# Optimization experiments

Hardware: AMD Instinct MI355X
Metric: run time of the kernel (lower is better)

Reference implementation:

```python
import jax, jax.numpy as jnp
import numpy as np


def setup_inputs() -> dict:
    key = jax.random.key(0)
    contour = jax.random.uniform(key, (200, 2), dtype=jnp.float32)  # coords in [0,1]
    return {"contour": contour, "size": 384}


def reference(contour, size):
    S = size
    eps = 1e-05
    k = 100000.0  # forward hardcodes k, ignoring self.k
    # mesh: (S^2, 1, 2), normalized pixel coordinates (torch.meshgrid default 'ij')
    grid = jnp.stack(jnp.meshgrid(jnp.arange(S), jnp.arange(S), indexing="ij"), axis=-1)
    mesh = (grid.reshape(-1, 2).astype(jnp.float32) / S)[:, None, :]
    diff = contour[None, :, :] - mesh                      # (S^2, N, 2)
    norm_diff = jnp.linalg.norm(diff, axis=-1)             # (S^2, N)
    min_diff = jnp.min(norm_diff, axis=1).reshape(S, S)    # distance to nearest vertex
    roll_diff = jnp.roll(diff, -1, axis=1)                 # next vertex diff
    # torch.roll(roll_diff, 1, dims=2) on a size-2 axis swaps x/y components
    cross = diff * roll_diff[..., ::-1]                    # (S^2, N, 2)
    sign = jnp.tanh(k * (cross[..., 1] - cross[..., 0]))   # smooth sign of 2D cross
    nd = jnp.clip(norm_diff, eps)
    nr = jnp.clip(jnp.linalg.norm(roll_diff, axis=-1), eps)
    cos_ang = jnp.clip(jnp.sum(diff * roll_diff, axis=-1) / (nd * nr), -1.0 + eps, 1.0 - eps)
    angles = jnp.arccos(cos_ang)                           # (S^2, N)
    winding = jnp.sum(sign * angles, axis=1) / (2.0 * jnp.pi)  # (S^2,)
    resize = winding.reshape(1, S, S)
    prod = resize * min_diff                               # (1, S, S)
    dmap = (prod / jnp.max(prod))[None]                    # (1, 1, S, S)
    return dmap
```

## Files before the change

kernel.cpp:

```cpp
#include <hip/hip_runtime.h>
#include <math.h>


#define INV_2PI 0.15915494309189535f
#define TWO_PI  6.28318530717958648f
#define PI_F    3.14159265358979323846f
#define HPI_F   1.57079632679489662f
#define KK2     200000.0f
#define CTHR    9e-5f

__device__ __forceinline__ float atan01(float q) {
    const float z = q * q;
    float p = fmaf(z,  0.0208351f, -0.0851330f);
    p = fmaf(z, p,  0.1801410f);
    p = fmaf(z, p, -0.3302995f);
    p = fmaf(z, p,  0.9998660f);
    return q * p;
}

__device__ __forceinline__ float corr_term(float ax_, float ay_, float bx_,
                                           float by_, float px, float py,
                                           float V) {
    const float dxc = ax_ - px, dyc = ay_ - py;
    const float dxn = bx_ - px, dyn = by_ - py;
    const float dot = fmaf(dxc, dxn, dyc * dyn);
    const float ay = fabsf(V), ax = fabsf(dot);
    const float mn = fminf(ax, ay), mx = fmaxf(ax, ay);
    const float q  = mn * __builtin_amdgcn_rcpf(fmaxf(mx, 1e-30f));
    float an = atan01(q);
    an = (ay > ax)    ? (HPI_F - an) : an;
    an = (dot < 0.0f) ? (PI_F - an)  : an;
    const float e = __expf(ay * -KK2);
    const float t = (1.0f - e) * __builtin_amdgcn_rcpf(1.0f + e);
    return (1.0f - t) * copysignf(an, -V);
}

__global__ void __launch_bounds__(256)
scan_kernel(const float2* __restrict__ c, int N, int S, float invS,
            float* __restrict__ wbuf) {
    __shared__ int   D[512];
    __shared__ float WC[512];
    __shared__ int   lst[16];
    __shared__ int   lcnt;

    const int tid = threadIdx.x;
    const int col = blockIdx.x;
    const float px = (float)col * invS;
    const float Sf = (float)S;

    for (int t = tid; t < 512; t += 256) { D[t] = 0; WC[t] = 0.0f; }
    if (tid == 0) lcnt = 0;
    __syncthreads();

    for (int n = tid; n < N; n += 256) {
        const float2 a = c[n];
        const float2 b = c[(n + 1 < N) ? (n + 1) : 0];
        const float EX = b.x - a.x;
        const float EY = b.y - a.y;
        const float Cc = a.x * b.y - a.y * b.x;
        const float W  = fmaf(-px, EY, Cc);

        const float ylo = fminf(a.y, b.y);
        const float yhi = fmaxf(a.y, b.y);
        const int s = (b.y > a.y) ? 1 : -1;
        int ja = (int)ceilf(ylo * Sf);
        int jb = (int)ceilf(yhi * Sf);
        ja = max(ja, 0); jb = min(jb, S);
        if (ja < jb) {
            const float Ga = (float)s * fmaf(EX, (float)ja * invS, W);
            const float Gb = (float)s * fmaf(EX, (float)(jb - 1) * invS, W);
            int j0 = ja, j1 = jb;
            if (Ga > 0.0f && Gb > 0.0f) {
            } else if (!(Ga > 0.0f) && !(Gb > 0.0f)) {
                j1 = j0;
            } else {
                const float r = -W / EX;
                const float rj = fminf(fmaxf(r * Sf, -1.0f), 386.0f);
                int jm = (int)ceilf(rj);
                jm = min(max(jm, ja), jb);
                if (Ga > 0.0f) j1 = jm; else j0 = jm;
            }
            if (j0 < j1) {
                atomicAdd(&D[j0],  s);
                atomicAdd(&D[j1], -s);
            }
        }

        const float aEX = fabsf(EX);
        if (aEX < 1e-12f) {
            if (fabsf(W) < CTHR) {
                const int k = atomicAdd(&lcnt, 1);
                if (k < 16) lst[k] = n;
            }
        } else {
            const float r  = -W / EX;
            const float dl = CTHR / aEX;
            float flo = (r - dl) * Sf;
            float fhi = (r + dl) * Sf;
            if (fhi >= 0.0f && flo <= Sf - 1.0f) {
                flo = fmaxf(flo, 0.0f);
                fhi = fminf(fhi, Sf - 1.0f);
                const int jl = (int)ceilf(flo);
                const int jh = (int)floorf(fhi);
                if (jh - jl > 12) {
                    const int k = atomicAdd(&lcnt, 1);
                    if (k < 16) lst[k] = n;
                } else {
                    for (int j = jl; j <= jh; ++j) {
                        const float py = (float)j * invS;
                        const float V = fmaf(EX, py, W);
                        if (fabsf(V) < CTHR)
                            atomicAdd(&WC[j],
                                      corr_term(a.x, a.y, b.x, b.y, px, py, V));
                    }
                }
            }
        }
    }
    __syncthreads();

    const int L = min(lcnt, 16);
    for (int k = 0; k < L; ++k) {
        const int n = lst[k];
        const float2 a = c[n];
        const float2 b = c[(n + 1 < N) ? (n + 1) : 0];
        const float EX = b.x - a.x;
        const float EY = b.y - a.y;
        const float W  = fmaf(-px, EY, a.x * b.y - a.y * b.x);
        for (int j = tid; j < S; j += 256) {
            const float py = (float)j * invS;
            const float V = fmaf(EX, py, W);
            if (fabsf(V) < CTHR)
                atomicAdd(&WC[j], corr_term(a.x, a.y, b.x, b.y, px, py, V));
        }
    }
    __syncthreads();

    #pragma unroll
    for (int off = 1; off < 512; off <<= 1) {
        const int j0 = tid, j1 = tid + 256;
        const int v0 = D[j0] + ((j0 >= off) ? D[j0 - off] : 0);
        const int v1 = D[j1] + ((j1 >= off) ? D[j1 - off] : 0);
        __syncthreads();
        D[j0] = v0; D[j1] = v1;
        __syncthreads();
    }

    for (int j = tid; j < S; j += 256)
        wbuf[col * S + j] = fmaf(-TWO_PI, (float)D[j], -WC[j]);
}

__global__ void __launch_bounds__(256)
prod_kernel(const float2* __restrict__ c, int N, int S, float invS,
            const float* __restrict__ wbuf, float* __restrict__ out,
            float* __restrict__ bmax) {
    __shared__ float2 sv[256];
    __shared__ int    scnt;
    __shared__ float  s_cd[4];
    __shared__ float  s_red[4];

    const int tid  = threadIdx.x;
    const int lane = tid & 63;
    const int wid  = tid >> 6;

    const int nbx = S >> 4;
    const int bi = blockIdx.x / nbx;
    const int bj = blockIdx.x - bi * nbx;
    const int i = (bi << 4) + (tid >> 4);
    const int j = (bj << 4) + (tid & 15);
    const float px = (float)i * invS, py = (float)j * invS;

    const float cx = ((float)(bi << 4) + 7.5f) * invS;
    const float cy = ((float)(bj << 4) + 7.5f) * invS;

    float cmin = 1e30f;
    for (int n = tid; n < N; n += 256) {
        const float2 v = c[n];
        const float dx = v.x - cx, dy = v.y - cy;
        cmin = fminf(cmin, fmaf(dx, dx, dy * dy));
    }
    #pragma unroll
    for (int off = 32; off >= 1; off >>= 1)
        cmin = fminf(cmin, __shfl_down(cmin, off, 64));
    if (lane == 0) s_cd[wid] = cmin;
    if (tid == 0) scnt = 0;
    __syncthreads();
    const float minc = fminf(fminf(s_cd[0], s_cd[1]), fminf(s_cd[2], s_cd[3]));

    const float T  = sqrtf(minc) + 0.0560f;
    const float T2 = T * T;

    for (int n = tid; n < N; n += 256) {
        const float2 v = c[n];
        const float dx = v.x - cx, dy = v.y - cy;
        if (fmaf(dx, dx, dy * dy) <= T2) {
            const int k = atomicAdd(&scnt, 1);
            sv[k] = v;
        }
    }
    __syncthreads();

    const int M = scnt;
    float minn = 1e30f;
    for (int k = 0; k < M; ++k) {
        const float2 v = sv[k];
        const float dx = v.x - px, dy = v.y - py;
        minn = fminf(minn, fmaf(dx, dx, dy * dy));
    }

    const int p = i * S + j;
    const float prod = (wbuf[p] * INV_2PI) * __builtin_amdgcn_sqrtf(minn);
    out[p] = prod;

    float v = prod;
    #pragma unroll
    for (int off = 32; off >= 1; off >>= 1)
        v = fmaxf(v, __shfl_down(v, off, 64));
    if (lane == 0) s_red[wid] = v;
    __syncthreads();
    if (tid == 0)
        bmax[blockIdx.x] = fmaxf(fmaxf(s_red[0], s_red[1]),
                                 fmaxf(s_red[2], s_red[3]));
}

__global__ void __launch_bounds__(256)
normalize_kernel(float4* __restrict__ out4, const float* __restrict__ bmax,
                 int nmax, int total4) {
    const int tid  = threadIdx.x;
    const int lane = tid & 63;
    const int wid  = tid >> 6;

    float m = -INFINITY;
    for (int t = tid; t < nmax; t += 256) m = fmaxf(m, bmax[t]);
    #pragma unroll
    for (int off = 32; off >= 1; off >>= 1)
        m = fmaxf(m, __shfl_down(m, off, 64));
    __shared__ float sm[4];
    if (lane == 0) sm[wid] = m;
    __syncthreads();
    m = fmaxf(fmaxf(sm[0], sm[1]), fmaxf(sm[2], sm[3]));
    const float inv = 1.0f / m;

    const int idx = blockIdx.x * 256 + tid;
    if (idx < total4) {
        float4 v = out4[idx];
        v.x *= inv; v.y *= inv; v.z *= inv; v.w *= inv;
        out4[idx] = v;
    }
}

extern "C" void kernel_launch(void* const* d_in, const int* in_sizes, int n_in,
                              void* d_out, int out_size, void* d_ws, size_t ws_size,
                              hipStream_t stream) {
    const float2* contour = (const float2*)d_in[0];
    const int N = in_sizes[0] / 2;
    const int S = (int)(sqrt((double)out_size) + 0.5);
    const float invS = 1.0f / (float)S;
    float* out  = (float*)d_out;
    float* bmax = (float*)d_ws;
    float* wbuf = (float*)((char*)d_ws + 16384);

    scan_kernel<<<S, 256, 0, stream>>>(contour, N, S, invS, wbuf);

    const int total  = S * S;
    const int pblocks = total / 256;
    prod_kernel<<<pblocks, 256, 0, stream>>>(contour, N, S, invS, wbuf,
                                             out, bmax);

    const int total4  = total / 4;
    const int nblocks = (total4 + 255) / 256;
    normalize_kernel<<<nblocks, 256, 0, stream>>>((float4*)out, bmax,
                                                  pblocks, total4);
}
```

Before: 64.21 us.

## Shrink scan kernel to single wavefront with shuffle-based prefix sum

The per-column scan kernel now runs with one 64-lane wavefront instead of 256 threads. The 18-barrier shared-memory Hillis-Steele scan over 512 entries is replaced by a per-lane sequential sum over 6 elements plus a wavefront shuffle scan, so only the two initial barriers remain. The threshold for deferring near-edge corrections to the cooperative list is raised to match the narrower block. The new layout hardcodes 6 entries per lane, so it assumes S is at most 384, and each block now walks the 200 edges with four times fewer threads.

```diff
diff --git a/kernel.cpp b/kernel.cpp
--- a/kernel.cpp
+++ b/kernel.cpp
@@ -35,24 +35,25 @@
     return (1.0f - t) * copysignf(an, -V);
 }
 
-__global__ void __launch_bounds__(256)
+__global__ void __launch_bounds__(64)
 scan_kernel(const float2* __restrict__ c, int N, int S, float invS,
             float* __restrict__ wbuf) {
-    __shared__ int   D[512];
-    __shared__ float WC[512];
+    __shared__ int   D[448];
+    __shared__ float WC[384];
     __shared__ int   lst[16];
     __shared__ int   lcnt;
 
-    const int tid = threadIdx.x;
-    const int col = blockIdx.x;
+    const int lane = threadIdx.x;
+    const int col  = blockIdx.x;
     const float px = (float)col * invS;
     const float Sf = (float)S;
 
-    for (int t = tid; t < 512; t += 256) { D[t] = 0; WC[t] = 0.0f; }
-    if (tid == 0) lcnt = 0;
-    __syncthreads();
-
-    for (int n = tid; n < N; n += 256) {
+    for (int t = lane; t < 448; t += 64) D[t] = 0;
+    for (int t = lane; t < 384; t += 64) WC[t] = 0.0f;
+    if (lane == 0) lcnt = 0;
+    __syncthreads();
+
+    for (int n = lane; n < N; n += 64) {
         const float2 a = c[n];
         const float2 b = c[(n + 1 < N) ? (n + 1) : 0];
         const float EX = b.x - a.x;
@@ -102,7 +103,7 @@
                 fhi = fminf(fhi, Sf - 1.0f);
                 const int jl = (int)ceilf(flo);
                 const int jh = (int)floorf(fhi);
-                if (jh - jl > 12) {
+                if (jh - jl > 24) {
                     const int k = atomicAdd(&lcnt, 1);
                     if (k < 16) lst[k] = n;
                 } else {
@@ -127,7 +128,7 @@
         const float EX = b.x - a.x;
         const float EY = b.y - a.y;
         const float W  = fmaf(-px, EY, a.x * b.y - a.y * b.x);
-        for (int j = tid; j < S; j += 256) {
+        for (int j = lane; j < S; j += 64) {
             const float py = (float)j * invS;
             const float V = fmaf(EX, py, W);
             if (fabsf(V) < CTHR)
@@ -136,18 +137,26 @@
     }
     __syncthreads();
 
-    #pragma unroll
-    for (int off = 1; off < 512; off <<= 1) {
-        const int j0 = tid, j1 = tid + 256;
-        const int v0 = D[j0] + ((j0 >= off) ? D[j0 - off] : 0);
-        const int v1 = D[j1] + ((j1 >= off) ? D[j1 - off] : 0);
-        __syncthreads();
-        D[j0] = v0; D[j1] = v1;
-        __syncthreads();
-    }
-
-    for (int j = tid; j < S; j += 256)
-        wbuf[col * S + j] = fmaf(-TWO_PI, (float)D[j], -WC[j]);
+    int d0 = D[6 * lane + 0], d1 = D[6 * lane + 1], d2 = D[6 * lane + 2];
+    int d3 = D[6 * lane + 3], d4 = D[6 * lane + 4], d5 = D[6 * lane + 5];
+    const int l0 = d0,      l1 = l0 + d1, l2 = l1 + d2;
+    const int l3 = l2 + d3, l4 = l3 + d4, l5 = l4 + d5;
+    int inc = l5;
+    #pragma unroll
+    for (int off = 1; off < 64; off <<= 1) {
+        const int y = __shfl_up(inc, off, 64);
+        if (lane >= off) inc += y;
+    }
+    const int excl = inc - l5;
+
+    const int jb6 = 6 * lane;
+    float* wrow = wbuf + col * S + jb6;
+    wrow[0] = fmaf(-TWO_PI, (float)(excl + l0), -WC[jb6 + 0]);
+    wrow[1] = fmaf(-TWO_PI, (float)(excl + l1), -WC[jb6 + 1]);
+    wrow[2] = fmaf(-TWO_PI, (float)(excl + l2), -WC[jb6 + 2]);
+    wrow[3] = fmaf(-TWO_PI, (float)(excl + l3), -WC[jb6 + 3]);
+    wrow[4] = fmaf(-TWO_PI, (float)(excl + l4), -WC[jb6 + 4]);
+    wrow[5] = fmaf(-TWO_PI, (float)(excl + l5), -WC[jb6 + 5]);
 }
 
 __global__ void __launch_bounds__(256)
@@ -260,7 +269,7 @@
     float* bmax = (float*)d_ws;
     float* wbuf = (float*)((char*)d_ws + 16384);
 
-    scan_kernel<<<S, 256, 0, stream>>>(contour, N, S, invS, wbuf);
+    scan_kernel<<<S, 64, 0, stream>>>(contour, N, S, invS, wbuf);
 
     const int total  = S * S;
     const int pblocks = total / 256;
```

New measurement: 66.02 us. +2.8%, slower.

## Fuse per-column winding scan into tiled product kernel, dropping intermediate buffer

Applied to the files above, without the earlier changes.

Merges the per-column winding-number scan kernel into the 16x16 tile kernel. Each tile now computes its own crossing differences and correction terms for its 16 columns, clipped to its 16 rows, and prefix-sums them in shared memory. The contour is staged once in LDS. This removes one launch and the global winding buffer round trip. In exchange, every tile re-walks all edges for its columns (16 rows of 16 threads per edge pass), which duplicates edge work across row tiles. It also assumes N<=256 for the shared staging.

```diff
diff --git a/kernel.cpp b/kernel.cpp
--- a/kernel.cpp
+++ b/kernel.cpp
@@ -35,125 +35,12 @@
     return (1.0f - t) * copysignf(an, -V);
 }
 
-__global__ void __launch_bounds__(256)
-scan_kernel(const float2* __restrict__ c, int N, int S, float invS,
-            float* __restrict__ wbuf) {
-    __shared__ int   D[512];
-    __shared__ float WC[512];
-    __shared__ int   lst[16];
-    __shared__ int   lcnt;
-
-    const int tid = threadIdx.x;
-    const int col = blockIdx.x;
-    const float px = (float)col * invS;
-    const float Sf = (float)S;
-
-    for (int t = tid; t < 512; t += 256) { D[t] = 0; WC[t] = 0.0f; }
-    if (tid == 0) lcnt = 0;
-    __syncthreads();
-
-    for (int n = tid; n < N; n += 256) {
-        const float2 a = c[n];
-        const float2 b = c[(n + 1 < N) ? (n + 1) : 0];
-        const float EX = b.x - a.x;
-        const float EY = b.y - a.y;
-        const float Cc = a.x * b.y - a.y * b.x;
-        const float W  = fmaf(-px, EY, Cc);
-
-        const float ylo = fminf(a.y, b.y);
-        const float yhi = fmaxf(a.y, b.y);
-        const int s = (b.y > a.y) ? 1 : -1;
-        int ja = (int)ceilf(ylo * Sf);
-        int jb = (int)ceilf(yhi * Sf);
-        ja = max(ja, 0); jb = min(jb, S);
-        if (ja < jb) {
-            const float Ga = (float)s * fmaf(EX, (float)ja * invS, W);
-            const float Gb = (float)s * fmaf(EX, (float)(jb - 1) * invS, W);
-            int j0 = ja, j1 = jb;
-            if (Ga > 0.0f && Gb > 0.0f) {
-            } else if (!(Ga > 0.0f) && !(Gb > 0.0f)) {
-                j1 = j0;
-            } else {
-                const float r = -W / EX;
-                const float rj = fminf(fmaxf(r * Sf, -1.0f), 386.0f);
-                int jm = (int)ceilf(rj);
-                jm = min(max(jm, ja), jb);
-                if (Ga > 0.0f) j1 = jm; else j0 = jm;
-            }
-            if (j0 < j1) {
-                atomicAdd(&D[j0],  s);
-                atomicAdd(&D[j1], -s);
-            }
-        }
-
-        const float aEX = fabsf(EX);
-        if (aEX < 1e-12f) {
-            if (fabsf(W) < CTHR) {
-                const int k = atomicAdd(&lcnt, 1);
-                if (k < 16) lst[k] = n;
-            }
-        } else {
-            const float r  = -W / EX;
-            const float dl = CTHR / aEX;
-            float flo = (r - dl) * Sf;
-            float fhi = (r + dl) * Sf;
-            if (fhi >= 0.0f && flo <= Sf - 1.0f) {
-                flo = fmaxf(flo, 0.0f);
-                fhi = fminf(fhi, Sf - 1.0f);
-                const int jl = (int)ceilf(flo);
-                const int jh = (int)floorf(fhi);
-                if (jh - jl > 12) {
-                    const int k = atomicAdd(&lcnt, 1);
-                    if (k < 16) lst[k] = n;
-                } else {
-                    for (int j = jl; j <= jh; ++j) {
-                        const float py = (float)j * invS;
-                        const float V = fmaf(EX, py, W);
-                        if (fabsf(V) < CTHR)
-                            atomicAdd(&WC[j],
-                                      corr_term(a.x, a.y, b.x, b.y, px, py, V));
-                    }
-                }
-            }
-        }
-    }
-    __syncthreads();
-
-    const int L = min(lcnt, 16);
-    for (int k = 0; k < L; ++k) {
-        const int n = lst[k];
-        const float2 a = c[n];
-        const float2 b = c[(n + 1 < N) ? (n + 1) : 0];
-        const float EX = b.x - a.x;
-        const float EY = b.y - a.y;
-        const float W  = fmaf(-px, EY, a.x * b.y - a.y * b.x);
-        for (int j = tid; j < S; j += 256) {
-            const float py = (float)j * invS;
-            const float V = fmaf(EX, py, W);
-            if (fabsf(V) < CTHR)
-                atomicAdd(&WC[j], corr_term(a.x, a.y, b.x, b.y, px, py, V));
-        }
-    }
-    __syncthreads();
-
-    #pragma unroll
-    for (int off = 1; off < 512; off <<= 1) {
-        const int j0 = tid, j1 = tid + 256;
-        const int v0 = D[j0] + ((j0 >= off) ? D[j0 - off] : 0);
-        const int v1 = D[j1] + ((j1 >= off) ? D[j1 - off] : 0);
-        __syncthreads();
-        D[j0] = v0; D[j1] = v1;
-        __syncthreads();
-    }
-
-    for (int j = tid; j < S; j += 256)
-        wbuf[col * S + j] = fmaf(-TWO_PI, (float)D[j], -WC[j]);
-}
-
-__global__ void __launch_bounds__(256)
-prod_kernel(const float2* __restrict__ c, int N, int S, float invS,
-            const float* __restrict__ wbuf, float* __restrict__ out,
-            float* __restrict__ bmax) {
+__global__ void __launch_bounds__(256, 4)
+tile_kernel(const float2* __restrict__ c, int N, int S, float invS,
+            float* __restrict__ out, float* __restrict__ bmax) {
+    __shared__ float2 sc[256];
+    __shared__ int    D[16][17];
+    __shared__ float  WC[16][16];
     __shared__ float2 sv[256];
     __shared__ int    scnt;
     __shared__ float  s_cd[4];
@@ -162,36 +49,110 @@
     const int tid  = threadIdx.x;
     const int lane = tid & 63;
     const int wid  = tid >> 6;
+    const float Sf = (float)S;
 
     const int nbx = S >> 4;
     const int bi = blockIdx.x / nbx;
     const int bj = blockIdx.x - bi * nbx;
-    const int i = (bi << 4) + (tid >> 4);
-    const int j = (bj << 4) + (tid & 15);
+    const int i0 = bi << 4;
+    const int jt = bj << 4;
+
+    if (tid < N) sc[tid] = c[tid];
+    for (int t = tid; t < 272; t += 256) ((int*)D)[t] = 0;
+    WC[tid >> 4][tid & 15] = 0.0f;
+    if (tid == 0) scnt = 0;
+    __syncthreads();
+
+    {
+        const int ci = tid & 15;
+        const float px = (float)(i0 + ci) * invS;
+        for (int n = tid >> 4; n < N; n += 16) {
+            const float2 a = sc[n];
+            const float2 b = sc[(n + 1 < N) ? (n + 1) : 0];
+            const float EX = b.x - a.x;
+            const float EY = b.y - a.y;
+            const float Cc = a.x * b.y - a.y * b.x;
+            const float W  = fmaf(-px, EY, Cc);
+
+            const float ylo = fminf(a.y, b.y);
+            const float yhi = fmaxf(a.y, b.y);
+            const int s = (b.y > a.y) ? 1 : -1;
+            int ja = (int)ceilf(ylo * Sf);
+            int jb = (int)ceilf(yhi * Sf);
+            ja = max(ja, 0); jb = min(jb, S);
+            if (ja < jb) {
+                const float Ga = (float)s * fmaf(EX, (float)ja * invS, W);
+                const float Gb = (float)s * fmaf(EX, (float)(jb - 1) * invS, W);
+                int j0 = ja, j1 = jb;
+                if (Ga > 0.0f && Gb > 0.0f) {
+                } else if (!(Ga > 0.0f) && !(Gb > 0.0f)) {
+                    j1 = j0;
+                } else {
+                    const float r = -W / EX;
+                    const float rj = fminf(fmaxf(r * Sf, -1.0f), 386.0f);
+                    int jm = (int)ceilf(rj);
+                    jm = min(max(jm, ja), jb);
+                    if (Ga > 0.0f) j1 = jm; else j0 = jm;
+                }
+                const int j0c = max(j0, jt);
+                const int j1c = min(j1, jt + 16);
+                if (j0c < j1c) {
+                    atomicAdd(&D[ci][j0c - jt],  s);
+                    atomicAdd(&D[ci][j1c - jt], -s);
+                }
+            }
+
+            const float aEX = fabsf(EX);
+            float flo, fhi;
+            if (aEX < 1e-12f) {
+                if (fabsf(W) < CTHR) { flo = (float)jt; fhi = (float)(jt + 15); }
+                else                 { flo = 1.0f;      fhi = 0.0f; }
+            } else {
+                const float r  = -W / EX;
+                const float dl = CTHR / aEX;
+                flo = (r - dl) * Sf;
+                fhi = (r + dl) * Sf;
+            }
+            flo = fmaxf(flo, (float)jt);
+            fhi = fminf(fhi, (float)(jt + 15));
+            if (flo <= fhi) {
+                const int jl = (int)ceilf(flo);
+                const int jh = (int)floorf(fhi);
+                for (int j = jl; j <= jh; ++j) {
+                    const float py = (float)j * invS;
+                    const float V = fmaf(EX, py, W);
+                    if (fabsf(V) < CTHR)
+                        atomicAdd(&WC[ci][j - jt],
+                                  corr_term(a.x, a.y, b.x, b.y, px, py, V));
+                }
+            }
+        }
+    }
+
+    const int i = i0 + (tid >> 4);
+    const int j = jt + (tid & 15);
     const float px = (float)i * invS, py = (float)j * invS;
-
-    const float cx = ((float)(bi << 4) + 7.5f) * invS;
-    const float cy = ((float)(bj << 4) + 7.5f) * invS;
+    const float cx = ((float)i0 + 7.5f) * invS;
+    const float cy = ((float)jt + 7.5f) * invS;
 
     float cmin = 1e30f;
-    for (int n = tid; n < N; n += 256) {
-        const float2 v = c[n];
+    if (tid < N) {
+        const float2 v = sc[tid];
         const float dx = v.x - cx, dy = v.y - cy;
-        cmin = fminf(cmin, fmaf(dx, dx, dy * dy));
+        cmin = fmaf(dx, dx, dy * dy);
     }
     #pragma unroll
     for (int off = 32; off >= 1; off >>= 1)
         cmin = fminf(cmin, __shfl_down(cmin, off, 64));
     if (lane == 0) s_cd[wid] = cmin;
-    if (tid == 0) scnt = 0;
-    __syncthreads();
+    __syncthreads();
+
     const float minc = fminf(fminf(s_cd[0], s_cd[1]), fminf(s_cd[2], s_cd[3]));
-
     const float T  = sqrtf(minc) + 0.0560f;
     const float T2 = T * T;
 
-    for (int n = tid; n < N; n += 256) {
-        const float2 v = c[n];
+    if (tid < N) {
+        const float2 v = sc[tid];
         const float dx = v.x - cx, dy = v.y - cy;
         if (fmaf(dx, dx, dy * dy) <= T2) {
             const int k = atomicAdd(&scnt, 1);
@@ -199,6 +160,14 @@
         }
     }
     __syncthreads();
+
+    const int cl = tid >> 4;
+    const int rl = tid & 15;
+    int wind = 0;
+    #pragma unroll
+    for (int q = 0; q < 16; ++q)
+        wind += (q <= rl) ? D[cl][q] : 0;
+    const float w = fmaf(-TWO_PI, (float)wind, -WC[cl][rl]);
 
     const int M = scnt;
     float minn = 1e30f;
@@ -209,7 +178,7 @@
     }
 
     const int p = i * S + j;
-    const float prod = (wbuf[p] * INV_2PI) * __builtin_amdgcn_sqrtf(minn);
+    const float prod = (w * INV_2PI) * __builtin_amdgcn_sqrtf(minn);
     out[p] = prod;
 
     float v = prod;
@@ -258,17 +227,13 @@
     const float invS = 1.0f / (float)S;
     float* out  = (float*)d_out;
     float* bmax = (float*)d_ws;
-    float* wbuf = (float*)((char*)d_ws + 16384);
-
-    scan_kernel<<<S, 256, 0, stream>>>(contour, N, S, invS, wbuf);
-
-    const int total  = S * S;
-    const int pblocks = total / 256;
-    prod_kernel<<<pblocks, 256, 0, stream>>>(contour, N, S, invS, wbuf,
-                                             out, bmax);
+
+    const int total   = S * S;
+    const int tblocks = total / 256;
+    tile_kernel<<<tblocks, 256, 0, stream>>>(contour, N, S, invS, out, bmax);
 
     const int total4  = total / 4;
     const int nblocks = (total4 + 255) / 256;
     normalize_kernel<<<nblocks, 256, 0, stream>>>((float4*)out, bmax,
-                                                  pblocks, total4);
-}
+                                                  tblocks, total4);
+}
```

Measured after the change: 67.89 us. +5.7%, slower.
